# Kernel optimization log

Hardware: AMD Instinct MI355X
Metric: run time of the kernel (lower is better)

## Reference

```python
import jax, jax.numpy as jnp
import numpy as np


def setup_inputs() -> dict:
    key = jax.random.key(0)
    ks = jax.random.split(key, 9)
    B, Lq, Lk, D = 8, 2048, 2048, 768
    s = 1.0 / np.sqrt(D)
    return {
        "queries": jax.random.normal(ks[0], (B, Lq, D), dtype=jnp.float32),
        "values": jax.random.normal(ks[1], (B, Lk, D), dtype=jnp.float32),
        "mask": jax.random.randint(ks[2], (B, Lq, Lk), 0, 2) > 0,
        "Wq": jax.random.normal(ks[3], (D, D), dtype=jnp.float32) * s,
        "bq": jax.random.normal(ks[4], (D,), dtype=jnp.float32) * s,
        "Wk": jax.random.normal(ks[5], (D, D), dtype=jnp.float32) * s,
        "bk": jax.random.normal(ks[6], (D,), dtype=jnp.float32) * s,
        "Wv": jax.random.normal(ks[7], (D, D), dtype=jnp.float32) * s,
        "bv": jax.random.normal(ks[8], (D,), dtype=jnp.float32) * s,
    }


def reference(queries, values, mask, Wq, bq, Wk, bk, Wv, bv):
    NEG = jnp.asarray(-1e9, queries.dtype)
    # torch Linear: x @ W.T + b
    q = jnp.einsum("bld,ed->ble", queries, Wq) + bq
    v = jnp.einsum("bld,ed->ble", values, Wv) + bv
    # NOTE (faithful to source): keys are the key-projection of the
    # already value-projected tensor.
    k = jnp.einsum("bld,ed->ble", v, Wk) + bk
    score = jnp.einsum("bqd,bkd->bqk", q, k)  # [B, Lq, Lk]
    score = jnp.where(mask, score, NEG)
    attn = jax.nn.sigmoid(score)  # sigmoid attention, no normalization
    context = jnp.einsum("bqk,bkd->bqd", attn, v)
    return context
```

## Files before the change

kernel.cpp:

```cpp
#include <hip/hip_runtime.h>
#include <hip/hip_bf16.h>

typedef __bf16 bf16_t;
typedef __bf16 bf16x8 __attribute__((ext_vector_type(8)));
typedef __bf16 bf16x4 __attribute__((ext_vector_type(4)));
typedef float  f32x4  __attribute__((ext_vector_type(4)));

#define LDS_DST(p) ((__attribute__((address_space(3))) void*)(p))
#define GLB_SRC(p) ((const __attribute__((address_space(1))) void*)(p))

#define SBAR()   asm volatile("s_barrier" ::: "memory")
#define WVM8()   asm volatile("s_waitcnt vmcnt(8)" ::: "memory")
#define WVM4()   asm volatile("s_waitcnt vmcnt(4)" ::: "memory")
#define WVM0()   asm volatile("s_waitcnt vmcnt(0)" ::: "memory")
#define SP1()    __builtin_amdgcn_s_setprio(1)
#define SP0()    __builtin_amdgcn_s_setprio(0)

__global__ void __launch_bounds__(256)
f32_to_bf16_kernel(const float* __restrict__ in, bf16_t* __restrict__ out, int n4) {
  int i = blockIdx.x * 256 + threadIdx.x;
  if (i < n4) {
    const float4 v = reinterpret_cast<const float4*>(in)[i];
    bf16x4 o;
    o[0] = (bf16_t)v.x; o[1] = (bf16_t)v.y; o[2] = (bf16_t)v.z; o[3] = (bf16_t)v.w;
    reinterpret_cast<bf16x4*>(out)[i] = o;
  }
}

__global__ void __launch_bounds__(256)
mask_pack_kernel(const int* __restrict__ mask, unsigned* __restrict__ bits) {
  const long i = (long)blockIdx.x * 256 + threadIdx.x;
  const int4* m4 = reinterpret_cast<const int4*>(mask + i * 32);
  unsigned w = 0;
#pragma unroll
  for (int j = 0; j < 8; ++j) {
    const int4 v = m4[j];
    w |= (v.x != 0 ? 1u : 0u) << (j * 4);
    w |= (v.y != 0 ? 2u : 0u) << (j * 4);
    w |= (v.z != 0 ? 4u : 0u) << (j * 4);
    w |= (v.w != 0 ? 8u : 0u) << (j * 4);
  }
  bits[i] = w;
}

__global__ void __launch_bounds__(256)
transpose_bf16_kernel(const bf16_t* __restrict__ in, bf16_t* __restrict__ out,
                      int R, int C) {
  __shared__ bf16_t tile[64][72];
  const long base = (long)blockIdx.z * R * C;
  const bf16_t* ib = in + base;
  bf16_t* ob = out + base;
  const int r0 = blockIdx.x * 64, c0 = blockIdx.y * 64;
  const int tid = threadIdx.x;
  const int rr = tid >> 3, cg = tid & 7;
#pragma unroll
  for (int p = 0; p < 2; ++p) {
    int row = p * 32 + rr;
    bf16x8 v = *reinterpret_cast<const bf16x8*>(ib + (long)(r0 + row) * C + c0 + cg * 8);
    *reinterpret_cast<bf16x8*>(&tile[row][cg * 8]) = v;
  }
  __syncthreads();
#pragma unroll
  for (int p = 0; p < 2; ++p) {
    int c = p * 32 + rr;
    bf16x8 v;
#pragma unroll
    for (int i = 0; i < 8; ++i) v[i] = tile[cg * 8 + i][c];
    *reinterpret_cast<bf16x8*>(ob + (long)(c0 + c) * R + r0 + cg * 8) = v;
  }
}


__device__ __forceinline__ void read_A(const char* smem, int off, bf16x8 (&af)[8], int xk0) {
#pragma unroll
  for (int mf = 0; mf < 4; ++mf)
#pragma unroll
    for (int kk = 0; kk < 2; ++kk)
      af[mf * 2 + kk] = *reinterpret_cast<const bf16x8*>(
          smem + off + mf * 2048 + (kk ? (xk0 ^ 64) : xk0));
}

__device__ __forceinline__ void read_B(const char* smem, int off, bf16x8 (&bf_)[4], int xk0) {
#pragma unroll
  for (int nf = 0; nf < 2; ++nf)
#pragma unroll
    for (int kk = 0; kk < 2; ++kk)
      bf_[nf * 2 + kk] = *reinterpret_cast<const bf16x8*>(
          smem + off + nf * 2048 + (kk ? (xk0 ^ 64) : xk0));
}

template <int MH, int NH>
__device__ __forceinline__ void mfma_q(const bf16x8 (&af)[8], const bf16x8 (&bf_)[4],
                                       f32x4 (&acc)[8][4]) {
#pragma unroll
  for (int mf = 0; mf < 4; ++mf)
#pragma unroll
    for (int nf = 0; nf < 2; ++nf)
#pragma unroll
      for (int kk = 0; kk < 2; ++kk)
        acc[MH * 4 + mf][NH * 2 + nf] = __builtin_amdgcn_mfma_f32_16x16x32_bf16(
            af[mf * 2 + kk], bf_[nf * 2 + kk], acc[MH * 4 + mf][NH * 2 + nf], 0, 0, 0);
}

#define STAGE_A(slot, mh, kt) do {                                            \
  _Pragma("unroll") for (int j_ = 0; j_ < 2; ++j_)                            \
    __builtin_amdgcn_global_load_lds(                                         \
        GLB_SRC(pA + (long)(j_ * 128 + (mh) * 64) * K + (kt)),                \
        LDS_DST(smem + (slot) * 65536 + (arow0 + j_ * 128 + (mh) * 64) * 128),\
        16, 0, 0);                                                            \
} while (0)

#define STAGE_B(slot, nh, kt) do {                                            \
  _Pragma("unroll") for (int j_ = 0; j_ < 2; ++j_)                            \
    __builtin_amdgcn_global_load_lds(                                         \
        GLB_SRC(pB + (long)(j_ * 128 + (nh) * 32) * K + (kt)),                \
        LDS_DST(smem + (slot) * 65536 + 32768 +                               \
                (brow0 + j_ * 128 + (nh) * 32) * 128),                        \
        16, 0, 0);                                                            \
} while (0)

template <int MODE>
__global__ void __launch_bounds__(512, 2)
gemm8p_kernel(const bf16_t* __restrict__ A, const bf16_t* __restrict__ B,
              const float* __restrict__ bias, const unsigned* __restrict__ maskbits,
              void* __restrict__ Cout, int M, int N, int K,
              long sA, long sB, long sC, long sMask) {
  __shared__ __align__(1024) char smem[131072];
  const int bz = blockIdx.z;
  const bf16_t* Ab = A + bz * sA;
  const bf16_t* Bb = B + bz * sB;
  const int bm = blockIdx.x * 256, bn = blockIdx.y * 256;
  const int tid = threadIdx.x;
  const int wave = tid >> 6, lane = tid & 63;
  const int wr = wave >> 2, wc = wave & 3;
  const int l15 = lane & 15, lg = lane >> 4;
  const int xk0 = (lg * 16) ^ ((lane & 7) << 4);
  const int NT = K >> 6;

  const int lr = lane >> 3;
  const int cgs = ((lane & 7) ^ lr) * 8;
  const int arow0 = wave * 8;
  const int brow0 = (wave >> 2) * 64 + (wave & 3) * 8;
  const bf16_t* pA = Ab + (long)(bm + arow0 + lr) * K + cgs;
  const bf16_t* pB = Bb + (long)(bn + brow0 + lr) * K + cgs;

  const int aoff = wr * 16384 + l15 * 128;
  const int boff = 32768 + wc * 8192 + l15 * 128;

  f32x4 acc[8][4] = {};
  bf16x8 afX[8], bfB[4], bf0[4];

  STAGE_A(0, 0, 0); STAGE_B(0, 0, 0); STAGE_B(0, 1, 0); STAGE_A(0, 1, 0);
  STAGE_A(1, 0, 64); STAGE_B(1, 0, 64);
  STAGE_B(1, 1, 64); STAGE_A(1, 1, 64);
  WVM8();
  SBAR();
  read_A(smem, aoff + 0, afX, xk0);
  read_B(smem, boff + 0, bf0, xk0);

  int slot = 0;
  for (int t = 0; t + 2 < NT; ++t) {
    const int so = slot * 65536, sn = (slot ^ 1) * 65536;
    const int k2 = (t + 2) << 6;
    read_B(smem, so + boff + 4096, bfB, xk0);
    STAGE_A(slot, 0, k2); STAGE_B(slot, 0, k2);
    SP1(); mfma_q<0, 0>(afX, bf0, acc); SP0();
    SP1(); mfma_q<0, 1>(afX, bfB, acc); SP0();
    read_A(smem, so + aoff + 8192, afX, xk0);
    WVM8(); SBAR();
    SP1(); mfma_q<1, 1>(afX, bfB, acc); SP0();
    SP1(); mfma_q<1, 0>(afX, bf0, acc); SP0();
    read_A(smem, sn + aoff + 0, afX, xk0);
    read_B(smem, sn + boff + 0, bf0, xk0);
    STAGE_B(slot, 1, k2); STAGE_A(slot, 1, k2);
    WVM8(); SBAR();
    slot ^= 1;
  }

  {
    const int so = slot * 65536, sn = (slot ^ 1) * 65536;
    read_B(smem, so + boff + 4096, bfB, xk0);
    SP1(); mfma_q<0, 0>(afX, bf0, acc); SP0();
    SP1(); mfma_q<0, 1>(afX, bfB, acc); SP0();
    read_A(smem, so + aoff + 8192, afX, xk0);
    WVM4(); SBAR();
    SP1(); mfma_q<1, 1>(afX, bfB, acc); SP0();
    SP1(); mfma_q<1, 0>(afX, bf0, acc); SP0();
    read_A(smem, sn + aoff + 0, afX, xk0);
    read_B(smem, sn + boff + 0, bf0, xk0);
    WVM0(); SBAR();
    read_B(smem, sn + boff + 4096, bfB, xk0);
    SP1(); mfma_q<0, 0>(afX, bf0, acc); SP0();
    SP1(); mfma_q<0, 1>(afX, bfB, acc); SP0();
    read_A(smem, sn + aoff + 8192, afX, xk0);
    SP1(); mfma_q<1, 1>(afX, bfB, acc); SP0();
    SP1(); mfma_q<1, 0>(afX, bf0, acc); SP0();
  }

  float* eb = (float*)smem;
  const int lrow = tid >> 3, t7 = tid & 7;
#pragma unroll
  for (int rd = 0; rd < 4; ++rd) {
    __syncthreads();
#pragma unroll
    for (int fi = 0; fi < 2; ++fi)
#pragma unroll
      for (int nf = 0; nf < 4; ++nf)
#pragma unroll
        for (int r = 0; r < 4; ++r) {
          const int lr2 = wr * 32 + fi * 16 + lg * 4 + r;
          eb[lr2 * 256 + wc * 64 + nf * 16 + l15] = acc[rd * 2 + fi][nf][r];
        }
    __syncthreads();
    const int growt = rd * 32 + lrow + ((lrow >> 5) * 96);
    const long rowbase = (long)(bm + growt) * N + bn;
    if constexpr (MODE == 1) {
      const unsigned* mw =
          maskbits + bz * sMask + (long)(bm + growt) * (N >> 5) + (bn >> 5);
      const uint4 w0 = *reinterpret_cast<const uint4*>(mw);
      const uint4 w1 = *reinterpret_cast<const uint4*>(mw + 4);
      const unsigned wq[8] = {w0.x, w0.y, w0.z, w0.w, w1.x, w1.y, w1.z, w1.w};
#pragma unroll
      for (int q = 0; q < 8; ++q) {
        const int c4 = (q * 8 + t7) * 4;
        const f32x4 v = *reinterpret_cast<const f32x4*>(&eb[lrow * 256 + c4]);
        const unsigned nib = (wq[q] >> (t7 * 4)) & 0xFu;
        bf16x4 o;
        o[0] = (bf16_t)((nib & 1u) ? 1.f / (1.f + __expf(-v[0])) : 0.f);
        o[1] = (bf16_t)((nib & 2u) ? 1.f / (1.f + __expf(-v[1])) : 0.f);
        o[2] = (bf16_t)((nib & 4u) ? 1.f / (1.f + __expf(-v[2])) : 0.f);
        o[3] = (bf16_t)((nib & 8u) ? 1.f / (1.f + __expf(-v[3])) : 0.f);
        *reinterpret_cast<bf16x4*>((bf16_t*)Cout + bz * sC + rowbase + c4) = o;
      }
    } else {
#pragma unroll
      for (int q = 0; q < 8; ++q) {
        const int c4 = (q * 8 + t7) * 4;
        const f32x4 v = *reinterpret_cast<const f32x4*>(&eb[lrow * 256 + c4]);
        if constexpr (MODE == 0) {
          const f32x4 b4 = *reinterpret_cast<const f32x4*>(bias + bn + c4);
          bf16x4 o;
          o[0] = (bf16_t)(v[0] + b4[0]); o[1] = (bf16_t)(v[1] + b4[1]);
          o[2] = (bf16_t)(v[2] + b4[2]); o[3] = (bf16_t)(v[3] + b4[3]);
          *reinterpret_cast<bf16x4*>((bf16_t*)Cout + bz * sC + rowbase + c4) = o;
        } else {
          *reinterpret_cast<f32x4*>((float*)Cout + bz * sC + rowbase + c4) = v;
        }
      }
    }
  }
}

extern "C" void kernel_launch(void* const* d_in, const int* in_sizes, int n_in,
                              void* d_out, int out_size, void* d_ws, size_t ws_size,
                              hipStream_t stream) {
  const float* queries = (const float*)d_in[0];
  const float* values  = (const float*)d_in[1];
  const int*   mask    = (const int*)d_in[2];
  const float* Wq = (const float*)d_in[3];
  const float* bq = (const float*)d_in[4];
  const float* Wk = (const float*)d_in[5];
  const float* bk = (const float*)d_in[6];
  const float* Wv = (const float*)d_in[7];
  const float* bv = (const float*)d_in[8];

  char* ws = (char*)d_ws;
  bf16_t* qb  = (bf16_t*)(ws + 0);
  bf16_t* vb  = (bf16_t*)(ws + 25165824);
  bf16_t* wqb = (bf16_t*)(ws + 50331648);
  bf16_t* wkb = (bf16_t*)(ws + 51511296);
  bf16_t* wvb = (bf16_t*)(ws + 52690944);
  bf16_t* qp  = (bf16_t*)(ws + 53870592);
  bf16_t* vp  = (bf16_t*)(ws + 79036416);
  bf16_t* kp  = (bf16_t*)(ws + 104202240);
  bf16_t* vpT = (bf16_t*)(ws + 129368064);
  bf16_t* P   = (bf16_t*)(ws + 154533888);
  unsigned* mbits = (unsigned*)(ws + 221642752);

  mask_pack_kernel<<<4096, 256, 0, stream>>>(mask, mbits);

  f32_to_bf16_kernel<<<12288, 256, 0, stream>>>(queries, qb, 3145728);
  f32_to_bf16_kernel<<<12288, 256, 0, stream>>>(values, vb, 3145728);
  f32_to_bf16_kernel<<<576, 256, 0, stream>>>(Wq, wqb, 147456);
  f32_to_bf16_kernel<<<576, 256, 0, stream>>>(Wk, wkb, 147456);
  f32_to_bf16_kernel<<<576, 256, 0, stream>>>(Wv, wvb, 147456);

  const dim3 blk2(512);

  gemm8p_kernel<0><<<dim3(64, 3, 1), blk2, 0, stream>>>(
      qb, wqb, bq, nullptr, qp, 16384, 768, 768, 0, 0, 0, 0);
  gemm8p_kernel<0><<<dim3(64, 3, 1), blk2, 0, stream>>>(
      vb, wvb, bv, nullptr, vp, 16384, 768, 768, 0, 0, 0, 0);
  gemm8p_kernel<0><<<dim3(64, 3, 1), blk2, 0, stream>>>(
      vp, wkb, bk, nullptr, kp, 16384, 768, 768, 0, 0, 0, 0);

  transpose_bf16_kernel<<<dim3(32, 12, 8), 256, 0, stream>>>(vp, vpT, 2048, 768);

  gemm8p_kernel<1><<<dim3(8, 8, 8), blk2, 0, stream>>>(
      qp, kp, nullptr, mbits, P, 2048, 2048, 768,
      (long)2048 * 768, (long)2048 * 768, (long)2048 * 2048, (long)2048 * 64);

  gemm8p_kernel<2><<<dim3(8, 3, 8), blk2, 0, stream>>>(
      P, vpT, nullptr, nullptr, d_out, 2048, 768, 2048,
      (long)2048 * 2048, (long)768 * 2048, (long)2048 * 768, 0);
}
```

Measured before the change: 292.9 us.

## Batch conversion and projection launches, ballot-pack mask, remap blocks across XCDs

Merges the float-to-bf16 conversions into two launches and runs the Q and V projections in a single launch using the z grid dimension. Rewrites mask packing so each wave reads the mask coalesced and packs it with a wave ballot. Adds an XCD-aware remapping of workgroup indices for L2 locality and swaps the sigmoid division for a hardware reciprocal. The cost is extra kernel arguments and branching on the pointers, plus slightly lower sigmoid precision.

New measurement: 271.8 us. -7.2%, faster.

```diff
diff --git a/kernel.cpp b/kernel.cpp
--- a/kernel.cpp
+++ b/kernel.cpp
@@ -17,7 +17,10 @@
 #define SP0()    __builtin_amdgcn_s_setprio(0)
 
 __global__ void __launch_bounds__(256)
-f32_to_bf16_kernel(const float* __restrict__ in, bf16_t* __restrict__ out, int n4) {
+conv2_kernel(const float* __restrict__ a, const float* __restrict__ b,
+             bf16_t* __restrict__ oa, bf16_t* __restrict__ ob, int n4) {
+  const float* in = blockIdx.z ? b : a;
+  bf16_t* out = blockIdx.z ? ob : oa;
   int i = blockIdx.x * 256 + threadIdx.x;
   if (i < n4) {
     const float4 v = reinterpret_cast<const float4*>(in)[i];
@@ -28,19 +31,36 @@
 }
 
 __global__ void __launch_bounds__(256)
-mask_pack_kernel(const int* __restrict__ mask, unsigned* __restrict__ bits) {
-  const long i = (long)blockIdx.x * 256 + threadIdx.x;
-  const int4* m4 = reinterpret_cast<const int4*>(mask + i * 32);
-  unsigned w = 0;
-#pragma unroll
-  for (int j = 0; j < 8; ++j) {
-    const int4 v = m4[j];
-    w |= (v.x != 0 ? 1u : 0u) << (j * 4);
-    w |= (v.y != 0 ? 2u : 0u) << (j * 4);
-    w |= (v.z != 0 ? 4u : 0u) << (j * 4);
-    w |= (v.w != 0 ? 8u : 0u) << (j * 4);
-  }
-  bits[i] = w;
+conv3_kernel(const float* __restrict__ a, const float* __restrict__ b,
+             const float* __restrict__ c, bf16_t* __restrict__ oa,
+             bf16_t* __restrict__ ob, bf16_t* __restrict__ oc, int n4) {
+  const float* in = blockIdx.z == 0 ? a : (blockIdx.z == 1 ? b : c);
+  bf16_t* out = blockIdx.z == 0 ? oa : (blockIdx.z == 1 ? ob : oc);
+  int i = blockIdx.x * 256 + threadIdx.x;
+  if (i < n4) {
+    const float4 v = reinterpret_cast<const float4*>(in)[i];
+    bf16x4 o;
+    o[0] = (bf16_t)v.x; o[1] = (bf16_t)v.y; o[2] = (bf16_t)v.z; o[3] = (bf16_t)v.w;
+    reinterpret_cast<bf16x4*>(out)[i] = o;
+  }
+}
+
+__global__ void __launch_bounds__(256)
+mask_pack_kernel(const int* __restrict__ mask, unsigned long long* __restrict__ bits) {
+  const long wid = (((long)blockIdx.x * 256 + threadIdx.x) >> 6);
+  const int lane = threadIdx.x & 63;
+  const long base = wid * 512;
+  unsigned long long b[8];
+#pragma unroll
+  for (int i = 0; i < 8; ++i) {
+    const int m = mask[base + i * 64 + lane];
+    b[i] = __ballot(m != 0);
+  }
+  if (lane == 0) {
+    unsigned long long* o = bits + wid * 8;
+#pragma unroll
+    for (int i = 0; i < 8; ++i) o[i] = b[i];
+  }
 }
 
 __global__ void __launch_bounds__(256)
@@ -124,12 +144,30 @@
 gemm8p_kernel(const bf16_t* __restrict__ A, const bf16_t* __restrict__ B,
               const float* __restrict__ bias, const unsigned* __restrict__ maskbits,
               void* __restrict__ Cout, int M, int N, int K,
-              long sA, long sB, long sC, long sMask) {
+              long sA, long sB, long sC, long sMask,
+              const bf16_t* __restrict__ A2, const bf16_t* __restrict__ B2,
+              const float* __restrict__ bias2, void* __restrict__ C2) {
   __shared__ __align__(1024) char smem[131072];
-  const int bz = blockIdx.z;
-  const bf16_t* Ab = A + bz * sA;
-  const bf16_t* Bb = B + bz * sB;
-  const int bm = blockIdx.x * 256, bn = blockIdx.y * 256;
+
+  const int gx = gridDim.x, gy = gridDim.y;
+  int flat = blockIdx.x + gx * (blockIdx.y + gy * blockIdx.z);
+  const int nwg = gx * gy * (int)gridDim.z;
+  const int q8 = nwg >> 3, r8 = nwg & 7;
+  const int xcd = flat & 7, idx = flat >> 3;
+  flat = (xcd < r8 ? xcd * (q8 + 1) : r8 * (q8 + 1) + (xcd - r8) * q8) + idx;
+  const int bxi = flat % gx; flat /= gx;
+  const int byi = flat % gy;
+  const int bz  = flat / gy;
+
+  const bf16_t* Ab; const bf16_t* Bb;
+  const float* biasp = bias; void* Cp = Cout;
+  if constexpr (MODE == 0) {
+    if (bz) { Ab = A2; Bb = B2; biasp = bias2; Cp = C2; }
+    else    { Ab = A;  Bb = B; }
+  } else {
+    Ab = A + bz * sA; Bb = B + bz * sB;
+  }
+  const int bm = bxi * 256, bn = byi * 256;
   const int tid = threadIdx.x;
   const int wave = tid >> 6, lane = tid & 63;
   const int wr = wave >> 2, wc = wave & 3;
@@ -226,11 +264,11 @@
         const f32x4 v = *reinterpret_cast<const f32x4*>(&eb[lrow * 256 + c4]);
         const unsigned nib = (wq[q] >> (t7 * 4)) & 0xFu;
         bf16x4 o;
-        o[0] = (bf16_t)((nib & 1u) ? 1.f / (1.f + __expf(-v[0])) : 0.f);
-        o[1] = (bf16_t)((nib & 2u) ? 1.f / (1.f + __expf(-v[1])) : 0.f);
-        o[2] = (bf16_t)((nib & 4u) ? 1.f / (1.f + __expf(-v[2])) : 0.f);
-        o[3] = (bf16_t)((nib & 8u) ? 1.f / (1.f + __expf(-v[3])) : 0.f);
-        *reinterpret_cast<bf16x4*>((bf16_t*)Cout + bz * sC + rowbase + c4) = o;
+        o[0] = (bf16_t)((nib & 1u) ? __builtin_amdgcn_rcpf(1.f + __expf(-v[0])) : 0.f);
+        o[1] = (bf16_t)((nib & 2u) ? __builtin_amdgcn_rcpf(1.f + __expf(-v[1])) : 0.f);
+        o[2] = (bf16_t)((nib & 4u) ? __builtin_amdgcn_rcpf(1.f + __expf(-v[2])) : 0.f);
+        o[3] = (bf16_t)((nib & 8u) ? __builtin_amdgcn_rcpf(1.f + __expf(-v[3])) : 0.f);
+        *reinterpret_cast<bf16x4*>((bf16_t*)Cp + bz * sC + rowbase + c4) = o;
       }
     } else {
 #pragma unroll
@@ -238,13 +276,13 @@
         const int c4 = (q * 8 + t7) * 4;
         const f32x4 v = *reinterpret_cast<const f32x4*>(&eb[lrow * 256 + c4]);
         if constexpr (MODE == 0) {
-          const f32x4 b4 = *reinterpret_cast<const f32x4*>(bias + bn + c4);
+          const f32x4 b4 = *reinterpret_cast<const f32x4*>(biasp + bn + c4);
           bf16x4 o;
           o[0] = (bf16_t)(v[0] + b4[0]); o[1] = (bf16_t)(v[1] + b4[1]);
           o[2] = (bf16_t)(v[2] + b4[2]); o[3] = (bf16_t)(v[3] + b4[3]);
-          *reinterpret_cast<bf16x4*>((bf16_t*)Cout + bz * sC + rowbase + c4) = o;
+          *reinterpret_cast<bf16x4*>((bf16_t*)Cp + bz * sC + rowbase + c4) = o;
         } else {
-          *reinterpret_cast<f32x4*>((float*)Cout + bz * sC + rowbase + c4) = v;
+          *reinterpret_cast<f32x4*>((float*)Cp + bz * sC + rowbase + c4) = v;
         }
       }
     }
@@ -275,32 +313,31 @@
   bf16_t* kp  = (bf16_t*)(ws + 104202240);
   bf16_t* vpT = (bf16_t*)(ws + 129368064);
   bf16_t* P   = (bf16_t*)(ws + 154533888);
-  unsigned* mbits = (unsigned*)(ws + 221642752);
-
-  mask_pack_kernel<<<4096, 256, 0, stream>>>(mask, mbits);
-
-  f32_to_bf16_kernel<<<12288, 256, 0, stream>>>(queries, qb, 3145728);
-  f32_to_bf16_kernel<<<12288, 256, 0, stream>>>(values, vb, 3145728);
-  f32_to_bf16_kernel<<<576, 256, 0, stream>>>(Wq, wqb, 147456);
-  f32_to_bf16_kernel<<<576, 256, 0, stream>>>(Wk, wkb, 147456);
-  f32_to_bf16_kernel<<<576, 256, 0, stream>>>(Wv, wvb, 147456);
+  unsigned long long* mbits = (unsigned long long*)(ws + 221642752);
+
+  mask_pack_kernel<<<16384, 256, 0, stream>>>(mask, mbits);
+
+  conv2_kernel<<<dim3(12288, 1, 2), 256, 0, stream>>>(queries, values, qb, vb, 3145728);
+  conv3_kernel<<<dim3(576, 1, 3), 256, 0, stream>>>(Wq, Wk, Wv, wqb, wkb, wvb, 147456);
 
   const dim3 blk2(512);
 
+  gemm8p_kernel<0><<<dim3(64, 3, 2), blk2, 0, stream>>>(
+      qb, wqb, bq, nullptr, qp, 16384, 768, 768, 0, 0, 0, 0,
+      vb, wvb, bv, vp);
   gemm8p_kernel<0><<<dim3(64, 3, 1), blk2, 0, stream>>>(
-      qb, wqb, bq, nullptr, qp, 16384, 768, 768, 0, 0, 0, 0);
-  gemm8p_kernel<0><<<dim3(64, 3, 1), blk2, 0, stream>>>(
-      vb, wvb, bv, nullptr, vp, 16384, 768, 768, 0, 0, 0, 0);
-  gemm8p_kernel<0><<<dim3(64, 3, 1), blk2, 0, stream>>>(
-      vp, wkb, bk, nullptr, kp, 16384, 768, 768, 0, 0, 0, 0);
+      vp, wkb, bk, nullptr, kp, 16384, 768, 768, 0, 0, 0, 0,
+      vp, wkb, bk, kp);
 
   transpose_bf16_kernel<<<dim3(32, 12, 8), 256, 0, stream>>>(vp, vpT, 2048, 768);
 
   gemm8p_kernel<1><<<dim3(8, 8, 8), blk2, 0, stream>>>(
-      qp, kp, nullptr, mbits, P, 2048, 2048, 768,
-      (long)2048 * 768, (long)2048 * 768, (long)2048 * 2048, (long)2048 * 64);
+      qp, kp, nullptr, (const unsigned*)mbits, P, 2048, 2048, 768,
+      (long)2048 * 768, (long)2048 * 768, (long)2048 * 2048, (long)2048 * 64,
+      nullptr, nullptr, nullptr, nullptr);
 
   gemm8p_kernel<2><<<dim3(8, 3, 8), blk2, 0, stream>>>(
       P, vpT, nullptr, nullptr, d_out, 2048, 768, 2048,
-      (long)2048 * 2048, (long)768 * 2048, (long)2048 * 768, 0);
-}
+      (long)2048 * 2048, (long)768 * 2048, (long)2048 * 768, 0,
+      nullptr, nullptr, nullptr, nullptr);
+}
```
